# Kernel tuning notes

Measured on AMD Instinct MI355X. Metric: run time of the kernel, lower is better.

The kernel has to match this reference:

```python
import jax, jax.numpy as jnp
import numpy as np

B, T, C, L = 512, 256, 256, 64  # batch, time, num_classes (blank = C-1), max label len
NEG = -1e30  # log-space "zero"
EPS = 1e-7   # keras K.epsilon()


def setup_inputs() -> dict:
    key = jax.random.key(0)
    k1, k2, k3, k4 = jax.random.split(key, 4)
    # y_pred are post-softmax probabilities (output of the recognizer head)
    y_pred = jax.nn.softmax(jax.random.normal(k1, (B, T, C), jnp.float32), axis=-1)
    labels = jax.random.randint(k2, (B, L), 0, C - 1, dtype=jnp.int32)  # exclude blank
    input_length = jax.random.randint(k3, (B, 1), T // 2, T + 1, dtype=jnp.int32)
    label_length = jax.random.randint(k4, (B, 1), 16, 49, dtype=jnp.int32)
    return {"y_pred": y_pred, "labels": labels,
            "input_length": input_length, "label_length": label_length}


def _ctc_batch_cost(y_pred, labels, input_length, label_length):
    # Faithful to K.ctc_batch_cost: blank = num_classes-1, loss = -log p(labels | y_pred).
    Bn, Tn, Cn = y_pred.shape
    Ln = labels.shape[1]
    S = 2 * Ln + 1
    blank = Cn - 1
    log_probs = jnp.log(y_pred + EPS)                      # [B,T,C]

    # Extended label sequence: blank, l1, blank, l2, ..., blank  -> [B,S]
    ext = jnp.full((Bn, S), blank, dtype=labels.dtype)
    ext = ext.at[:, 1::2].set(labels)

    # Skip transition (s-2 -> s) allowed iff ext[s] != blank and ext[s] != ext[s-2]
    same2 = jnp.concatenate(
        [jnp.ones((Bn, 2), bool), ext[:, 2:] == ext[:, :-2]], axis=1)
    allow_skip = (ext != blank) & ~same2                   # [B,S]

    # Emission log-probs gathered along the extended sequence: [B,T,S]
    emit = jnp.take_along_axis(log_probs, jnp.broadcast_to(ext[:, None, :], (Bn, Tn, S)), axis=2)

    # alpha at t=0: can start at first blank or first label
    alpha0 = jnp.full((Bn, S), NEG, dtype=log_probs.dtype)
    alpha0 = alpha0.at[:, 0].set(emit[:, 0, 0])
    alpha0 = alpha0.at[:, 1].set(emit[:, 0, 1])

    def shift1(a):
        return jnp.concatenate([jnp.full((Bn, 1), NEG, a.dtype), a[:, :-1]], axis=1)

    def step(alpha, xs):
        emit_t, active = xs                                # [B,S], [B,1] bool
        a1 = shift1(alpha)
        a2 = shift1(a1)
        a2 = jnp.where(allow_skip, a2, NEG)
        new = jax.nn.logsumexp(jnp.stack([alpha, a1, a2]), axis=0) + emit_t
        new = jnp.where(active, new, alpha)                # freeze past input_length
        return new, None

    emits = jnp.transpose(emit, (1, 0, 2))[1:]             # [T-1,B,S]
    active = jnp.arange(1, Tn)[:, None, None] < input_length[None, :, :]  # [T-1,B,1]
    alpha_T, _ = jax.lax.scan(step, alpha0, (emits, active))

    # Terminal states: last label (s = 2*ll-1) or final blank (s = 2*ll)
    ll = label_length[:, 0]
    idx = jnp.stack([2 * ll - 1, 2 * ll], axis=1)          # [B,2]
    final = jnp.take_along_axis(alpha_T, idx, axis=1)
    return -jax.nn.logsumexp(final, axis=1, keepdims=True)  # [B,1]


def reference(y_pred, labels, input_length, label_length):
    return _ctc_batch_cost(y_pred, labels, input_length, label_length)
```

## Files before the change

### kernel.cpp

```cpp
#include <hip/hip_runtime.h>

#define TT 256
#define CC 256
#define LLAB 64
#define NEGF -1e30f
#define EPSF 1e-7f
#define CH 16
#define NSLOT 4

__device__ __forceinline__ float lse2f(float a, float b) {
    float m = fmaxf(a, b);
    return m + __logf(__expf(a - m) + __expf(b - m));
}
__device__ __forceinline__ float lse3f(float a, float b, float c) {
    float m = fmaxf(fmaxf(a, b), c);
    return m + __logf(__expf(a - m) + __expf(b - m) + __expf(c - m));
}

__device__ __forceinline__ float wave_shr1(float x) {
    int r = __builtin_amdgcn_update_dpp(__float_as_int(NEGF), __float_as_int(x),
                                        0x138, 0xF, 0xF, false);
    return __int_as_float(r);
}

extern "C" __global__ __launch_bounds__(128) void ctc_fwd(
    const float* __restrict__ y_pred,
    const int* __restrict__ labels,
    const int* __restrict__ input_length,
    const int* __restrict__ label_length,
    float* __restrict__ out)
{
    const int b   = blockIdx.x;
    const int l   = threadIdx.x & 63;
    const int wid = threadIdx.x >> 6;

    __shared__ float lab_lds[NSLOT][CH][LLAB];
    __shared__ float blank_lds[NSLOT][CH];

    int len = input_length[b];
    len = len < 1 ? 1 : (len > TT ? TT : len);
    const int tmax = len - 1;
    const int nch  = (len - 1 + CH - 1) / CH;

    const int lab = labels[b * LLAB + l];
    const float* __restrict__ yp = y_pred + (size_t)b * (TT * CC);
    const float* __restrict__ pl = yp + lab;
    const float* __restrict__ pb = yp + (CC - 1);

    float s0 = NEGF, s1 = NEGF, s2 = NEGF;
    bool skip_ok = false;

    float labA[CH], labB[CH], blA = 0.f, blB = 0.f;

#define ISSUE(c, labv, blv)                                                  \
    {                                                                        \
        const int t0 = 1 + (c) * CH;                                         \
        _Pragma("unroll")                                                    \
        for (int j = 0; j < CH; ++j) {                                       \
            int t = t0 + j; t = t > tmax ? tmax : t;                         \
            labv[j] = pl[t * CC];                                            \
        }                                                                    \
        { int t = t0 + (l & 15); t = t > tmax ? tmax : t;                    \
          blv = pb[t * CC]; }                                                \
    }

#define FINISH(c, labv, blv)                                                 \
    {                                                                        \
        const int slot_ = (c) % NSLOT;                                       \
        float lg_ = __logf((blv) + EPSF);                                    \
        if (l < CH) blank_lds[slot_][l] = lg_;                               \
        _Pragma("unroll")                                                    \
        for (int j = 0; j < CH; ++j)                                         \
            lab_lds[slot_][j][l] = __logf(labv[j] + EPSF);                   \
    }

    if (wid == 1) {
        ISSUE(0, labB, blB);
        ISSUE(1, labA, blA);
        FINISH(0, labB, blB);
    } else {
        const int labp = __shfl_up(lab, 1);
        skip_ok = (l >= 1) && (lab != labp);
        if (l == 0) {
            s0 = __logf(pb[0] + EPSF);
            s1 = __logf(pl[0] + EPSF);
        }
    }
    __syncthreads();

    for (int k = 0; k < nch; ++k) {
        if (wid == 1) {
            if ((k & 1) == 0) { ISSUE(k + 2, labB, blB); FINISH(k + 1, labA, blA); }
            else              { ISSUE(k + 2, labA, blA); FINISH(k + 1, labB, blB); }
        } else {
            const int slot = k % NSLOT;
            float e[CH], bb[CH];
#pragma unroll
            for (int j = 0; j < CH; ++j) {
                e[j]  = lab_lds[slot][j][l];
                bb[j] = blank_lds[slot][j];
            }
#pragma unroll
            for (int j = 0; j < CH; ++j) {
                const int t = 1 + k * CH + j;
                float am1 = wave_shr1(s1);
                float n0 = lse2f(s0, am1) + bb[j];
                float n1 = lse3f(s1, s0, skip_ok ? am1 : NEGF) + e[j];
                float n2 = lse2f(s2, s1) + bb[j];
                const bool act = t < len;
                s0 = act ? n0 : s0;
                s1 = act ? n1 : s1;
                s2 = act ? n2 : s2;
            }
        }
        __syncthreads();
    }

    if (wid == 0) {
        int ll = label_length[b];
        ll = ll < 1 ? 1 : (ll > LLAB ? LLAB : ll);
        float v1 = __shfl(s1, ll - 1);
        float v2 = (ll < LLAB) ? __shfl(s0, ll) : __shfl(s2, 63);
        if (l == 0) out[b] = -lse2f(v1, v2);
    }
}

extern "C" void kernel_launch(void* const* d_in, const int* in_sizes, int n_in,
                              void* d_out, int out_size, void* d_ws, size_t ws_size,
                              hipStream_t stream) {
    (void)n_in; (void)out_size; (void)d_ws; (void)ws_size;
    const float* y_pred       = (const float*)d_in[0];
    const int*   labels       = (const int*)d_in[1];
    const int*   input_length = (const int*)d_in[2];
    const int*   label_length = (const int*)d_in[3];
    float* out = (float*)d_out;

    const int B = in_sizes[2];
    ctc_fwd<<<dim3(B), dim3(128), 0, stream>>>(y_pred, labels, input_length, label_length, out);
}
```

Measured before the change: 207.3 us.

## Run CTC alpha recursion in scaled linear space instead of log space

Replaces the log-sum-exp recursion with a linear-probability recursion that uses only adds and multiplies, renormalizing every four steps by a power of two taken from a wave-wide max and tracking the exponent in an integer accumulator. The producer wave stores probabilities plus epsilon rather than their logs, and skips loads for lanes past the label length. Chunk size goes to 32 with two LDS slots. This removes the many exp/log calls on the serial critical path, at the cost of a periodic wave max reduction and some risk of underflow between rescales.

```diff
diff --git a/kernel.cpp b/kernel.cpp
--- a/kernel.cpp
+++ b/kernel.cpp
@@ -3,24 +3,24 @@
 #define TT 256
 #define CC 256
 #define LLAB 64
-#define NEGF -1e30f
 #define EPSF 1e-7f
-#define CH 16
-#define NSLOT 4
+#define CH 32
+#define NSLOT 2
+#define LN2F 0.69314718055994531f
 
-__device__ __forceinline__ float lse2f(float a, float b) {
-    float m = fmaxf(a, b);
-    return m + __logf(__expf(a - m) + __expf(b - m));
-}
-__device__ __forceinline__ float lse3f(float a, float b, float c) {
-    float m = fmaxf(fmaxf(a, b), c);
-    return m + __logf(__expf(a - m) + __expf(b - m) + __expf(c - m));
+__device__ __forceinline__ float wave_shr1_zero(float x) {
+    int r = __builtin_amdgcn_update_dpp(0, __float_as_int(x), 0x138, 0xF, 0xF, false);
+    return __int_as_float(r);
 }
 
-__device__ __forceinline__ float wave_shr1(float x) {
-    int r = __builtin_amdgcn_update_dpp(__float_as_int(NEGF), __float_as_int(x),
-                                        0x138, 0xF, 0xF, false);
-    return __int_as_float(r);
+__device__ __forceinline__ float wave_max64(float x) {
+#define DSTEP(ctrl)                                                            \
+    { int t_ = __builtin_amdgcn_update_dpp(__float_as_int(x), __float_as_int(x),\
+                                           (ctrl), 0xF, 0xF, false);           \
+      x = fmaxf(x, __int_as_float(t_)); }
+    DSTEP(0x111) DSTEP(0x112) DSTEP(0x114) DSTEP(0x118) DSTEP(0x142) DSTEP(0x143)
+#undef DSTEP
+    return __int_as_float(__builtin_amdgcn_readlane(__float_as_int(x), 63));
 }
 
 extern "C" __global__ __launch_bounds__(128) void ctc_fwd(
@@ -42,58 +42,62 @@
     const int tmax = len - 1;
     const int nch  = (len - 1 + CH - 1) / CH;
 
-    const int lab = labels[b * LLAB + l];
+    int llm = label_length[b];
+    llm = llm < 1 ? 1 : (llm > LLAB ? LLAB : llm);
+
+    const int  lab   = labels[b * LLAB + l];
+    const bool ldlab = (l < llm);
+
     const float* __restrict__ yp = y_pred + (size_t)b * (TT * CC);
     const float* __restrict__ pl = yp + lab;
     const float* __restrict__ pb = yp + (CC - 1);
 
-    float s0 = NEGF, s1 = NEGF, s2 = NEGF;
-    bool skip_ok = false;
+    float s0 = 0.f, s1 = 0.f, s2 = 0.f, skipf = 0.f;
+    int   eacc = 0;
 
     float labA[CH], labB[CH], blA = 0.f, blB = 0.f;
 
 #define ISSUE(c, labv, blv)                                                  \
-    {                                                                        \
+    if ((c) < nch) {                                                         \
         const int t0 = 1 + (c) * CH;                                         \
         _Pragma("unroll")                                                    \
         for (int j = 0; j < CH; ++j) {                                       \
             int t = t0 + j; t = t > tmax ? tmax : t;                         \
-            labv[j] = pl[t * CC];                                            \
+            labv[j] = ldlab ? pl[t * CC] : 0.f;                              \
         }                                                                    \
-        { int t = t0 + (l & 15); t = t > tmax ? tmax : t;                    \
+        { int t = t0 + (l & (CH - 1)); t = t > tmax ? tmax : t;              \
           blv = pb[t * CC]; }                                                \
     }
 
 #define FINISH(c, labv, blv)                                                 \
-    {                                                                        \
-        const int slot_ = (c) % NSLOT;                                       \
-        float lg_ = __logf((blv) + EPSF);                                    \
-        if (l < CH) blank_lds[slot_][l] = lg_;                               \
+    if ((c) < nch) {                                                         \
+        const int slot_ = (c) & (NSLOT - 1);                                 \
+        if (l < CH) blank_lds[slot_][l] = blv + EPSF;                        \
         _Pragma("unroll")                                                    \
         for (int j = 0; j < CH; ++j)                                         \
-            lab_lds[slot_][j][l] = __logf(labv[j] + EPSF);                   \
+            lab_lds[slot_][j][l] = ldlab ? (labv[j] + EPSF) : 0.f;           \
     }
 
     if (wid == 1) {
-        ISSUE(0, labB, blB);
-        ISSUE(1, labA, blA);
-        FINISH(0, labB, blB);
+        ISSUE(0, labA, blA);
+        ISSUE(1, labB, blB);
+        FINISH(0, labA, blA);
     } else {
         const int labp = __shfl_up(lab, 1);
-        skip_ok = (l >= 1) && (lab != labp);
+        skipf = (l >= 1 && lab != labp) ? 1.f : 0.f;
         if (l == 0) {
-            s0 = __logf(pb[0] + EPSF);
-            s1 = __logf(pl[0] + EPSF);
+            s0 = pb[0] + EPSF;
+            s1 = pl[0] + EPSF;
         }
     }
     __syncthreads();
 
     for (int k = 0; k < nch; ++k) {
         if (wid == 1) {
-            if ((k & 1) == 0) { ISSUE(k + 2, labB, blB); FINISH(k + 1, labA, blA); }
-            else              { ISSUE(k + 2, labA, blA); FINISH(k + 1, labB, blB); }
+            if ((k & 1) == 0) { ISSUE(k + 2, labA, blA); FINISH(k + 1, labB, blB); }
+            else              { ISSUE(k + 2, labB, blB); FINISH(k + 1, labA, blA); }
         } else {
-            const int slot = k % NSLOT;
+            const int slot = k & (NSLOT - 1);
             float e[CH], bb[CH];
 #pragma unroll
             for (int j = 0; j < CH; ++j) {
@@ -103,25 +107,32 @@
 #pragma unroll
             for (int j = 0; j < CH; ++j) {
                 const int t = 1 + k * CH + j;
-                float am1 = wave_shr1(s1);
-                float n0 = lse2f(s0, am1) + bb[j];
-                float n1 = lse3f(s1, s0, skip_ok ? am1 : NEGF) + e[j];
-                float n2 = lse2f(s2, s1) + bb[j];
+                float am1 = wave_shr1_zero(s1);
+                float n0 = (s0 + am1) * bb[j];
+                float n1 = fmaf(am1, skipf, s1 + s0) * e[j];
+                float n2 = (s2 + s1) * bb[j];
                 const bool act = t < len;
                 s0 = act ? n0 : s0;
                 s1 = act ? n1 : s1;
                 s2 = act ? n2 : s2;
+                if ((j & 3) == 3) {
+                    float m = wave_max64(fmaxf(fmaxf(s0, s1), s2));
+                    int me = __float_as_int(m) >> 23;
+                    me = me < 26 ? 26 : me;
+                    float scale = __int_as_float((253 - me) << 23);
+                    s0 *= scale; s1 *= scale; s2 *= scale;
+                    eacc += me - 126;
+                }
             }
         }
         __syncthreads();
     }
 
     if (wid == 0) {
-        int ll = label_length[b];
-        ll = ll < 1 ? 1 : (ll > LLAB ? LLAB : ll);
-        float v1 = __shfl(s1, ll - 1);
-        float v2 = (ll < LLAB) ? __shfl(s0, ll) : __shfl(s2, 63);
-        if (l == 0) out[b] = -lse2f(v1, v2);
+        float v1 = __shfl(s1, llm - 1);
+        float v2 = (llm < LLAB) ? __shfl(s0, llm) : __shfl(s2, 63);
+        float v  = fmaxf(v1 + v2, 1e-37f);
+        if (l == 0) out[b] = -(__logf(v) + (float)eacc * LN2F);
     }
 }
 
```

After: 192.6 us. 1.08x faster.
